# Performance work log

Measured on AMD Instinct MI355X. Metric: run time of the kernel, lower is better.

The kernel has to match this reference:

```python
import jax, jax.numpy as jnp
import numpy as np

NUM_HEADS = 4
NUM_GROUPS = 8
EPS = 1e-5


def group_norm(x, w, b):
    # x: (B, C, H, W); normalize per group of C//NUM_GROUPS channels
    B, C, H, W = x.shape
    xg = x.reshape(B, NUM_GROUPS, C // NUM_GROUPS, H, W)
    mean = xg.mean(axis=(2, 3, 4), keepdims=True)
    var = xg.var(axis=(2, 3, 4), keepdims=True)
    xn = ((xg - mean) * jax.lax.rsqrt(var + EPS)).reshape(B, C, H, W)
    return xn * w[None, :, None, None] + b[None, :, None, None]


def conv1x1(x, w, b):
    # x: (B, C_in, H, W), w: (C_out, C_in), b: (C_out,)
    return jnp.einsum('bchw,oc->bohw', x, w) + b[None, :, None, None]


def setup_inputs() -> dict:
    key = jax.random.key(0)
    B, C, H, W = 4, 256, 64, 64
    k1, k2, k3 = jax.random.split(key, 3)
    scale = 1.0 / np.sqrt(C)
    return {
        'x': jax.random.normal(k1, (B, C, H, W), dtype=jnp.float32),
        'norm_w': jnp.ones((C,), dtype=jnp.float32),
        'norm_b': jnp.zeros((C,), dtype=jnp.float32),
        'qkv_w': jax.random.normal(k2, (3 * C, C), dtype=jnp.float32) * scale,
        'qkv_b': jnp.zeros((3 * C,), dtype=jnp.float32),
        'proj_w': jax.random.normal(k3, (C, C), dtype=jnp.float32) * scale,
        'proj_b': jnp.zeros((C,), dtype=jnp.float32),
    }


def reference(x, norm_w, norm_b, qkv_w, qkv_b, proj_w, proj_b):
    B, C, H, W = x.shape
    hd = C // NUM_HEADS  # head dim
    h = group_norm(x, norm_w, norm_b)
    qkv = conv1x1(h, qkv_w, qkv_b)            # (B, 3C, H, W)
    q, k, v = jnp.split(qkv, 3, axis=1)
    q = q.reshape(B, NUM_HEADS, hd, H * W)
    k = k.reshape(B, NUM_HEADS, hd, H * W)
    v = v.reshape(B, NUM_HEADS, hd, H * W)
    attn = jnp.einsum('bhcn,bhcm->bhnm', q, k) / jnp.sqrt(jnp.asarray(hd, x.dtype))
    attn = jax.nn.softmax(attn, axis=-1)
    out = jnp.einsum('bhnm,bhcm->bhcn', attn, v).reshape(B, C, H, W)
    out = conv1x1(out, proj_w, proj_b)
    return x + out
```

## Files before the change

kernel.cpp:

```cpp
#include <hip/hip_runtime.h>
#include <hip/hip_bf16.h>
#include <stdint.h>


#define B_  4
#define C_  256
#define N_  4096
#define NH_ 4
#define HD_ 64
#define G_  8
#define CPG_ 32
#define GRP_ELEMS (CPG_ * N_)

typedef __attribute__((ext_vector_type(8))) short short8;
typedef __attribute__((ext_vector_type(4))) float f32x4;
typedef __attribute__((ext_vector_type(4))) unsigned short us4;

__device__ __forceinline__ unsigned short f2bf(float f) {
  union { float f; unsigned u; } v; v.f = f;
  unsigned r = v.u + 0x7FFFu + ((v.u >> 16) & 1u);
  return (unsigned short)(r >> 16);
}

__device__ __forceinline__ unsigned pkbf2(float a, float b) {
  __hip_bfloat162 h = __float22bfloat162_rn(make_float2(a, b));
  unsigned r; __builtin_memcpy(&r, &h, sizeof(r)); return r;
}

__device__ __forceinline__ void dma16(const unsigned short* g, unsigned short* l) {
  __builtin_amdgcn_global_load_lds(
      (const __attribute__((address_space(1))) unsigned int*)(g),
      (__attribute__((address_space(3))) unsigned int*)(l), 16, 0, 0);
}

__global__ void gn_partial_cvt(const float* __restrict__ x, float* __restrict__ partial,
                               const float* __restrict__ qkvw, const float* __restrict__ projw,
                               unsigned short* __restrict__ wq, unsigned short* __restrict__ wp) {
  __shared__ float ls[8];
  int t = threadIdx.x;
  if (blockIdx.x >= 512) {
    int i = (blockIdx.x - 512) * 256 + t;
    if (i < 768 * 256) wq[i] = f2bf(qkvw[i]);
    if (i < 256 * 256) wp[i] = f2bf(projw[i]);
    return;
  }
  int idx = blockIdx.x;
  int slice = idx & 15, g = (idx >> 4) & 7, b = idx >> 7;
  const float* base = x + (size_t)(b * C_ + g * CPG_) * N_ + slice * 256;
  float s = 0.f, sq = 0.f;
#pragma unroll
  for (int cc = 0; cc < CPG_; cc++) {
    float v = base[(size_t)cc * N_ + t];
    s += v; sq += v * v;
  }
#pragma unroll
  for (int off = 32; off; off >>= 1) {
    s  += __shfl_down(s,  off, 64);
    sq += __shfl_down(sq, off, 64);
  }
  int wave = t >> 6, lane = t & 63;
  if (lane == 0) { ls[wave * 2] = s; ls[wave * 2 + 1] = sq; }
  __syncthreads();
  if (t == 0) {
    float S = ls[0] + ls[2] + ls[4] + ls[6];
    float SQ = ls[1] + ls[3] + ls[5] + ls[7];
    partial[idx * 2] = S; partial[idx * 2 + 1] = SQ;
  }
}

__global__ void gn_apply(const float* __restrict__ x,
                         const float* __restrict__ nw, const float* __restrict__ nb,
                         const float* __restrict__ partial, unsigned short* __restrict__ hT) {
  int nt = blockIdx.x, ct = blockIdx.y, b = blockIdx.z;
  __shared__ unsigned short tile[32][72];
  int t = threadIdx.x;
  int lane = t & 63;
  int grp = b * G_ + ct;
  float s = 0.f, sq = 0.f;
  if (lane < 16) {
    s  = partial[(grp * 16 + lane) * 2];
    sq = partial[(grp * 16 + lane) * 2 + 1];
  }
#pragma unroll
  for (int off = 8; off; off >>= 1) {
    s  += __shfl_down(s,  off, 64);
    sq += __shfl_down(sq, off, 64);
  }
  s  = __shfl(s,  0, 64);
  sq = __shfl(sq, 0, 64);
  const float inv = 1.0f / (float)GRP_ELEMS;
  float mean = s * inv;
  float rstd = rsqrtf(sq * inv - mean * mean + 1e-5f);

  int n_loc = t & 63, c_loc = t >> 6;
  const float* xb = x + (size_t)(b * C_ + ct * CPG_) * N_ + nt * 64;
#pragma unroll
  for (int rr = 0; rr < 8; rr++) {
    int cc = rr * 4 + c_loc;
    int c = ct * CPG_ + cc;
    float v = xb[(size_t)cc * N_ + n_loc];
    v = (v - mean) * rstd * nw[c] + nb[c];
    tile[cc][n_loc] = f2bf(v);
  }
  __syncthreads();
  int c2 = t & 31, n2 = t >> 5;
  unsigned short* out = hT + ((size_t)(b * N_ + nt * 64)) * C_ + ct * CPG_ + c2;
#pragma unroll
  for (int pass = 0; pass < 8; pass++) {
    int n = pass * 8 + n2;
    out[(size_t)n * C_] = tile[c2][n];
  }
}

__global__ __launch_bounds__(256) void qkv_gemm(
    const unsigned short* __restrict__ hT, const unsigned short* __restrict__ wq,
    const float* __restrict__ qb,
    unsigned short* __restrict__ Qt, unsigned short* __restrict__ Kt,
    unsigned short* __restrict__ V) {
  int ot = blockIdx.x >> 7;
  int nt = (blockIdx.x & 127) >> 2;
  int b  = blockIdx.x & 3;
  int t = threadIdx.x;
  int wave = t >> 6, lane = t & 63, l15 = lane & 15, quad = lane >> 4, l7 = l15 & 7;
  int o_base = ot * 64 + wave * 16;

  __shared__ __align__(16) unsigned short sh[128 * C_];
  {
    int row0 = wave * 2 + (lane >> 5);
    int col8 = lane & 31;
    int src8 = (col8 & 24) | ((col8 & 7) ^ (row0 & 7));
    const unsigned short* gsrc = hT + ((size_t)(b * N_ + nt * 128 + row0)) * C_ + src8 * 8;
#pragma unroll
    for (int it = 0; it < 16; it++)
      dma16(gsrc + (size_t)it * 8 * C_, sh + (it * 8 + wave * 2) * C_);
  }

  f32x4 acc[8];
#pragma unroll
  for (int tt = 0; tt < 8; tt++) acc[tt] = (f32x4){0.f, 0.f, 0.f, 0.f};

  const short8* arow = reinterpret_cast<const short8*>(wq + (size_t)(o_base + l15) * C_);

  asm volatile("s_waitcnt vmcnt(0)" ::: "memory");
  __syncthreads();

#pragma unroll
  for (int kk = 0; kk < 8; kk++) {
    short8 a = arow[kk * 4 + quad];
    int g = kk * 4 + quad;
    int col8 = (g & 24) | ((g & 7) ^ l7);
#pragma unroll
    for (int tt = 0; tt < 8; tt++) {
      short8 bf = *reinterpret_cast<const short8*>(&sh[(tt * 16 + l15) * C_ + col8 * 8]);
      acc[tt] = __builtin_amdgcn_mfma_f32_16x16x32_bf16(a, bf, acc[tt], 0, 0, 0);
    }
  }

  int sec = ot >> 2, head = ot & 3;
  int cw = wave * 16 + quad * 4;
  int bh = b * NH_ + head;
  const float SC = 0.125f * 1.44269504088896340736f;

  if (sec == 0) {
#pragma unroll
    for (int tt = 0; tt < 8; tt++) {
      int n = nt * 128 + tt * 16 + l15;
      us4 pk;
#pragma unroll
      for (int i = 0; i < 4; i++)
        pk[i] = f2bf((acc[tt][i] + qb[ot * 64 + cw + i]) * SC);
      *reinterpret_cast<us4*>(Qt + ((size_t)bh * N_ + n) * HD_ + cw) = pk;
    }
  } else if (sec == 1) {
#pragma unroll
    for (int tt = 0; tt < 8; tt++) {
      int n = nt * 128 + tt * 16 + l15;
      us4 pk;
#pragma unroll
      for (int i = 0; i < 4; i++)
        pk[i] = f2bf(acc[tt][i] + qb[ot * 64 + cw + i]);
      *reinterpret_cast<us4*>(Kt + ((size_t)bh * N_ + n) * HD_ + cw) = pk;
    }
  } else {
#pragma unroll
    for (int tt = 0; tt < 8; tt++) {
      int n = nt * 128 + tt * 16 + l15;
#pragma unroll
      for (int i = 0; i < 4; i++)
        V[((size_t)bh * HD_ + cw + i) * N_ + n] = f2bf(acc[tt][i] + qb[ot * 64 + cw + i]);
    }
  }
}

__global__ __launch_bounds__(256, 2) void flash_attn(
    const unsigned short* __restrict__ Qt, const unsigned short* __restrict__ Kt,
    const unsigned short* __restrict__ Vv, unsigned short* __restrict__ aoT) {
  int bh = blockIdx.x & 15, qt = blockIdx.x >> 4;
  int b = bh >> 2, head = bh & 3;
  int t = threadIdx.x;
  int wave = t >> 6, lane = t & 63, l15 = lane & 15, quad = lane >> 4;
  int l7 = l15 & 7;
  int qsub = wave >> 1, khalf = wave & 1;

  const unsigned short* Qb = Qt + (size_t)bh * N_ * HD_;
  const unsigned short* Kb = Kt + (size_t)bh * N_ * HD_;
  const unsigned short* Vb = Vv + (size_t)bh * HD_ * N_;
  int q_base = qt * 128 + qsub * 64;

  __shared__ __align__(16) unsigned char smem[74752];
  unsigned short* Ks = (unsigned short*)smem;
  unsigned short* Vs = (unsigned short*)(smem + 32768);
  unsigned short* Ps = (unsigned short*)(smem + 65536);
  float* Obuf = (float*)smem;
  float* lbuf = (float*)(smem + 34816);

  const short8 vones = {(short)0x3F80, (short)0x3F80, (short)0x3F80, (short)0x3F80,
                        (short)0x3F80, (short)0x3F80, (short)0x3F80, (short)0x3F80};

  short8 qf[4][2];
#pragma unroll
  for (int r = 0; r < 4; r++)
#pragma unroll
    for (int h = 0; h < 2; h++)
      qf[r][h] = *reinterpret_cast<const short8*>(
          Qb + (size_t)(q_base + r * 16 + l15) * HD_ + h * 32 + quad * 8);

  f32x4 oa[4][4], la[4];
#pragma unroll
  for (int r = 0; r < 4; r++) {
    la[r] = (f32x4){0.f, 0.f, 0.f, 0.f};
#pragma unroll
    for (int ct = 0; ct < 4; ct++) oa[r][ct] = (f32x4){0.f, 0.f, 0.f, 0.f};
  }

  int i8 = lane >> 3, e = lane & 7;
  int perm = (e ^ i8) * 8;
  int kvoff = (khalf * 2) * 4096;
  auto stage = [&](int kt2, int buf) {
    int m0 = khalf * 2048 + kt2 * 64;
    unsigned short* Kd = Ks + kvoff + buf * 4096;
    unsigned short* Vd = Vs + kvoff + buf * 4096;
#pragma unroll
    for (int cc = 0; cc < 4; cc++) {
      int c = qsub * 4 + cc;
      dma16(Kb + (size_t)(m0 + c * 8 + i8) * HD_ + perm, Kd + c * 512);
      dma16(Vb + (size_t)(c * 8 + i8) * N_ + m0 + perm, Vd + c * 512);
    }
  };

  stage(0, 0);

  unsigned short* Pw = Ps + wave * 16 * 72;

#pragma unroll 1
  for (int kt = 0; kt < 32; kt++) {
    int buf = kt & 1;
    if (kt + 1 < 32) {
      stage(kt + 1, buf ^ 1);
      asm volatile("s_waitcnt vmcnt(8)" ::: "memory");
    } else {
      asm volatile("s_waitcnt vmcnt(0)" ::: "memory");
    }
    __builtin_amdgcn_s_barrier();

    const unsigned short* Kbuf = Ks + kvoff + buf * 4096;
    const unsigned short* Vbuf = Vs + kvoff + buf * 4096;

    short8 kf[4][2], vf[4][2];
#pragma unroll
    for (int tt = 0; tt < 4; tt++)
#pragma unroll
      for (int kh2 = 0; kh2 < 2; kh2++) {
        kf[tt][kh2] = *reinterpret_cast<const short8*>(
            &Kbuf[(tt * 16 + l15) * 64 + (((kh2 * 4 + quad) ^ l7) * 8)]);
        vf[tt][kh2] = *reinterpret_cast<const short8*>(
            &Vbuf[(tt * 16 + l15) * 64 + (((kh2 * 4 + quad) ^ l7) * 8)]);
      }

#pragma unroll
    for (int r = 0; r < 4; r++) {
      f32x4 s[4];
#pragma unroll
      for (int tt = 0; tt < 4; tt++) {
        f32x4 z = (f32x4){0.f, 0.f, 0.f, 0.f};
        z = __builtin_amdgcn_mfma_f32_16x16x32_bf16(kf[tt][0], qf[r][0], z, 0, 0, 0);
        s[tt] = __builtin_amdgcn_mfma_f32_16x16x32_bf16(kf[tt][1], qf[r][1], z, 0, 0, 0);
      }
#pragma unroll
      for (int tt = 0; tt < 4; tt++) {
        union { unsigned u2[2]; us4 v; } w;
        w.u2[0] = pkbf2(__builtin_amdgcn_exp2f(s[tt][0]), __builtin_amdgcn_exp2f(s[tt][1]));
        w.u2[1] = pkbf2(__builtin_amdgcn_exp2f(s[tt][2]), __builtin_amdgcn_exp2f(s[tt][3]));
        *reinterpret_cast<us4*>(&Pw[l15 * 72 + tt * 16 + quad * 4]) = w.v;
      }
      short8 pf0 = *reinterpret_cast<const short8*>(&Pw[l15 * 72 + quad * 8]);
      short8 pf1 = *reinterpret_cast<const short8*>(&Pw[l15 * 72 + 32 + quad * 8]);
#pragma unroll
      for (int ct = 0; ct < 4; ct++) {
        oa[r][ct] = __builtin_amdgcn_mfma_f32_16x16x32_bf16(vf[ct][0], pf0, oa[r][ct], 0, 0, 0);
        oa[r][ct] = __builtin_amdgcn_mfma_f32_16x16x32_bf16(vf[ct][1], pf1, oa[r][ct], 0, 0, 0);
      }
      la[r] = __builtin_amdgcn_mfma_f32_16x16x32_bf16(vones, pf0, la[r], 0, 0, 0);
      la[r] = __builtin_amdgcn_mfma_f32_16x16x32_bf16(vones, pf1, la[r], 0, 0, 0);
    }
  }

  __builtin_amdgcn_s_barrier();
  if (khalf == 1) {
#pragma unroll
    for (int r = 0; r < 4; r++) {
#pragma unroll
      for (int ct = 0; ct < 4; ct++)
#pragma unroll
        for (int i = 0; i < 4; i++)
          Obuf[qsub * 4352 + (ct * 16 + quad * 4 + i) * 68 + r * 16 + l15] = oa[r][ct][i];
      if (quad == 0) lbuf[qsub * 64 + r * 16 + l15] = la[r][0];
    }
  }
  __builtin_amdgcn_s_barrier();
  if (khalf == 0) {
#pragma unroll
    for (int r = 0; r < 4; r++) {
      float inv = 1.0f / (la[r][0] + lbuf[qsub * 64 + r * 16 + l15]);
      int n = q_base + r * 16 + l15;
#pragma unroll
      for (int ct = 0; ct < 4; ct++) {
        const float* ob = &Obuf[qsub * 4352 + (ct * 16 + quad * 4) * 68 + r * 16 + l15];
        union { unsigned u2[2]; us4 v; } w;
        w.u2[0] = pkbf2((oa[r][ct][0] + ob[0]) * inv, (oa[r][ct][1] + ob[68]) * inv);
        w.u2[1] = pkbf2((oa[r][ct][2] + ob[136]) * inv, (oa[r][ct][3] + ob[204]) * inv);
        *reinterpret_cast<us4*>(
            aoT + ((size_t)(b * N_ + n)) * C_ + head * HD_ + ct * 16 + quad * 4) = w.v;
      }
    }
  }
}

__global__ __launch_bounds__(256) void proj_gemm(
    const unsigned short* __restrict__ aoT, const unsigned short* __restrict__ wp,
    const float* __restrict__ pb, const float* __restrict__ x,
    float* __restrict__ out) {
  int ot = blockIdx.x >> 7;
  int nt = (blockIdx.x & 127) >> 2;
  int b  = blockIdx.x & 3;
  int t = threadIdx.x;
  int wave = t >> 6, lane = t & 63, l15 = lane & 15, quad = lane >> 4, l7 = l15 & 7;
  int o_base = ot * 64 + wave * 16;

  __shared__ __align__(16) unsigned short sh[128 * C_];
  {
    int row0 = wave * 2 + (lane >> 5);
    int col8 = lane & 31;
    int src8 = (col8 & 24) | ((col8 & 7) ^ (row0 & 7));
    const unsigned short* gsrc = aoT + ((size_t)(b * N_ + nt * 128 + row0)) * C_ + src8 * 8;
#pragma unroll
    for (int it = 0; it < 16; it++)
      dma16(gsrc + (size_t)it * 8 * C_, sh + (it * 8 + wave * 2) * C_);
  }

  f32x4 acc[8];
#pragma unroll
  for (int tt = 0; tt < 8; tt++) acc[tt] = (f32x4){0.f, 0.f, 0.f, 0.f};

  const short8* arow = reinterpret_cast<const short8*>(wp + (size_t)(o_base + l15) * C_);

  asm volatile("s_waitcnt vmcnt(0)" ::: "memory");
  __syncthreads();

#pragma unroll
  for (int kk = 0; kk < 8; kk++) {
    short8 a = arow[kk * 4 + quad];
    int g = kk * 4 + quad;
    int col8 = (g & 24) | ((g & 7) ^ l7);
#pragma unroll
    for (int tt = 0; tt < 8; tt++) {
      short8 bf = *reinterpret_cast<const short8*>(&sh[(tt * 16 + l15) * C_ + col8 * 8]);
      acc[tt] = __builtin_amdgcn_mfma_f32_16x16x32_bf16(a, bf, acc[tt], 0, 0, 0);
    }
  }
#pragma unroll
  for (int tt = 0; tt < 8; tt++) {
    int n = nt * 128 + tt * 16 + l15;
#pragma unroll
    for (int i = 0; i < 4; i++) {
      int o = o_base + quad * 4 + i;
      size_t idx = ((size_t)(b * C_ + o)) * N_ + n;
      out[idx] = acc[tt][i] + pb[o] + x[idx];
    }
  }
}

extern "C" void kernel_launch(void* const* d_in, const int* in_sizes, int n_in,
                              void* d_out, int out_size, void* d_ws, size_t ws_size,
                              hipStream_t stream) {
  const float* x      = (const float*)d_in[0];
  const float* norm_w = (const float*)d_in[1];
  const float* norm_b = (const float*)d_in[2];
  const float* qkv_w  = (const float*)d_in[3];
  const float* qkv_b  = (const float*)d_in[4];
  const float* proj_w = (const float*)d_in[5];
  const float* proj_b = (const float*)d_in[6];
  float* out = (float*)d_out;

  char* ws = (char*)d_ws;
  size_t off = 0;
  auto alloc = [&](size_t bytes) { size_t o = off; off = (off + bytes + 255) & ~(size_t)255; return o; };
  size_t off_partial = alloc(512 * 2 * sizeof(float));
  size_t off_stats   = alloc(32 * 2 * sizeof(float));
  size_t off_wq      = alloc((size_t)768 * 256 * 2);
  size_t off_wp      = alloc((size_t)256 * 256 * 2);
  size_t off_hT      = alloc((size_t)B_ * N_ * C_ * 2);
  size_t off_Qt      = alloc((size_t)B_ * NH_ * N_ * HD_ * 2);
  size_t off_Kt      = alloc((size_t)B_ * NH_ * N_ * HD_ * 2);
  size_t off_V       = alloc((size_t)B_ * NH_ * HD_ * N_ * 2);
  size_t off_aoT     = alloc((size_t)B_ * N_ * C_ * 2);
  (void)off_stats;

  float* partial = (float*)(ws + off_partial);
  unsigned short* wq  = (unsigned short*)(ws + off_wq);
  unsigned short* wp  = (unsigned short*)(ws + off_wp);
  unsigned short* hT  = (unsigned short*)(ws + off_hT);
  unsigned short* Qt  = (unsigned short*)(ws + off_Qt);
  unsigned short* Kt  = (unsigned short*)(ws + off_Kt);
  unsigned short* V   = (unsigned short*)(ws + off_V);
  unsigned short* aoT = (unsigned short*)(ws + off_aoT);

  gn_partial_cvt<<<1280, 256, 0, stream>>>(x, partial, qkv_w, proj_w, wq, wp);
  gn_apply<<<dim3(64, 8, 4), 256, 0, stream>>>(x, norm_w, norm_b, partial, hT);
  qkv_gemm<<<1536, 256, 0, stream>>>(hT, wq, qkv_b, Qt, Kt, V);
  flash_attn<<<512, 256, 0, stream>>>(Qt, Kt, V, aoT);
  proj_gemm<<<512, 256, 0, stream>>>(aoT, wp, proj_b, x, out);
}
```

Baseline: 193.3 us.

## Double QKV GEMM output tile per block and vectorize gn_apply stores

The QKV GEMM now computes 128 output channels per block instead of 64, with each wave handling two 16-row A fragments that share B fragments read once from LDS. This halves the grid and the number of redundant hT tile loads into shared memory. In exchange it uses more accumulator registers per thread. Separately, gn_apply's transposed write-out now has each thread emit 8 contiguous bf16 values as two 8-byte stores instead of scattered 2-byte stores.

```diff
diff --git a/kernel.cpp b/kernel.cpp
--- a/kernel.cpp
+++ b/kernel.cpp
@@ -103,13 +103,15 @@
     tile[cc][n_loc] = f2bf(v);
   }
   __syncthreads();
-  int c2 = t & 31, n2 = t >> 5;
-  unsigned short* out = hT + ((size_t)(b * N_ + nt * 64)) * C_ + ct * CPG_ + c2;
-#pragma unroll
-  for (int pass = 0; pass < 8; pass++) {
-    int n = pass * 8 + n2;
-    out[(size_t)n * C_] = tile[c2][n];
-  }
+  int n = t >> 2, c8 = (t & 3) * 8;
+  us4 lo, hi;
+#pragma unroll
+  for (int j = 0; j < 4; j++) lo[j] = tile[c8 + j][n];
+#pragma unroll
+  for (int j = 0; j < 4; j++) hi[j] = tile[c8 + 4 + j][n];
+  unsigned short* outp = hT + ((size_t)(b * N_ + nt * 64 + n)) * C_ + ct * CPG_ + c8;
+  *reinterpret_cast<us4*>(outp) = lo;
+  *reinterpret_cast<us4*>(outp + 4) = hi;
 }
 
 __global__ __launch_bounds__(256) void qkv_gemm(
@@ -122,7 +124,6 @@
   int b  = blockIdx.x & 3;
   int t = threadIdx.x;
   int wave = t >> 6, lane = t & 63, l15 = lane & 15, quad = lane >> 4, l7 = l15 & 7;
-  int o_base = ot * 64 + wave * 16;
 
   __shared__ __align__(16) unsigned short sh[128 * C_];
   {
@@ -135,59 +136,76 @@
       dma16(gsrc + (size_t)it * 8 * C_, sh + (it * 8 + wave * 2) * C_);
   }
 
-  f32x4 acc[8];
-#pragma unroll
-  for (int tt = 0; tt < 8; tt++) acc[tt] = (f32x4){0.f, 0.f, 0.f, 0.f};
-
-  const short8* arow = reinterpret_cast<const short8*>(wq + (size_t)(o_base + l15) * C_);
+  f32x4 acc[2][8];
+#pragma unroll
+  for (int r = 0; r < 2; r++)
+#pragma unroll
+    for (int tt = 0; tt < 8; tt++) acc[r][tt] = (f32x4){0.f, 0.f, 0.f, 0.f};
+
+  const short8* arow[2];
+#pragma unroll
+  for (int r = 0; r < 2; r++)
+    arow[r] = reinterpret_cast<const short8*>(
+        wq + (size_t)(ot * 128 + wave * 32 + r * 16 + l15) * C_);
 
   asm volatile("s_waitcnt vmcnt(0)" ::: "memory");
   __syncthreads();
 
 #pragma unroll
   for (int kk = 0; kk < 8; kk++) {
-    short8 a = arow[kk * 4 + quad];
     int g = kk * 4 + quad;
     int col8 = (g & 24) | ((g & 7) ^ l7);
-#pragma unroll
-    for (int tt = 0; tt < 8; tt++) {
-      short8 bf = *reinterpret_cast<const short8*>(&sh[(tt * 16 + l15) * C_ + col8 * 8]);
-      acc[tt] = __builtin_amdgcn_mfma_f32_16x16x32_bf16(a, bf, acc[tt], 0, 0, 0);
-    }
-  }
-
-  int sec = ot >> 2, head = ot & 3;
-  int cw = wave * 16 + quad * 4;
+    short8 bfr[8];
+#pragma unroll
+    for (int tt = 0; tt < 8; tt++)
+      bfr[tt] = *reinterpret_cast<const short8*>(&sh[(tt * 16 + l15) * C_ + col8 * 8]);
+#pragma unroll
+    for (int r = 0; r < 2; r++) {
+      short8 a = arow[r][g];
+#pragma unroll
+      for (int tt = 0; tt < 8; tt++)
+        acc[r][tt] = __builtin_amdgcn_mfma_f32_16x16x32_bf16(a, bfr[tt], acc[r][tt], 0, 0, 0);
+    }
+  }
+
+  int sec = ot >> 1;
+  int head = (ot & 1) * 2 + (wave >> 1);
   int bh = b * NH_ + head;
   const float SC = 0.125f * 1.44269504088896340736f;
 
-  if (sec == 0) {
-#pragma unroll
-    for (int tt = 0; tt < 8; tt++) {
-      int n = nt * 128 + tt * 16 + l15;
-      us4 pk;
-#pragma unroll
-      for (int i = 0; i < 4; i++)
-        pk[i] = f2bf((acc[tt][i] + qb[ot * 64 + cw + i]) * SC);
-      *reinterpret_cast<us4*>(Qt + ((size_t)bh * N_ + n) * HD_ + cw) = pk;
-    }
-  } else if (sec == 1) {
-#pragma unroll
-    for (int tt = 0; tt < 8; tt++) {
-      int n = nt * 128 + tt * 16 + l15;
-      us4 pk;
-#pragma unroll
-      for (int i = 0; i < 4; i++)
-        pk[i] = f2bf(acc[tt][i] + qb[ot * 64 + cw + i]);
-      *reinterpret_cast<us4*>(Kt + ((size_t)bh * N_ + n) * HD_ + cw) = pk;
-    }
-  } else {
-#pragma unroll
-    for (int tt = 0; tt < 8; tt++) {
-      int n = nt * 128 + tt * 16 + l15;
-#pragma unroll
-      for (int i = 0; i < 4; i++)
-        V[((size_t)bh * HD_ + cw + i) * N_ + n] = f2bf(acc[tt][i] + qb[ot * 64 + cw + i]);
+#pragma unroll
+  for (int r = 0; r < 2; r++) {
+    int o_glob = ot * 128 + wave * 32 + r * 16;
+    int cw = (o_glob & 63) + quad * 4;
+    if (sec == 0) {
+#pragma unroll
+      for (int tt = 0; tt < 8; tt++) {
+        int n = nt * 128 + tt * 16 + l15;
+        us4 pk;
+#pragma unroll
+        for (int i = 0; i < 4; i++)
+          pk[i] = f2bf((acc[r][tt][i] + qb[o_glob + quad * 4 + i]) * SC);
+        *reinterpret_cast<us4*>(Qt + ((size_t)bh * N_ + n) * HD_ + cw) = pk;
+      }
+    } else if (sec == 1) {
+#pragma unroll
+      for (int tt = 0; tt < 8; tt++) {
+        int n = nt * 128 + tt * 16 + l15;
+        us4 pk;
+#pragma unroll
+        for (int i = 0; i < 4; i++)
+          pk[i] = f2bf(acc[r][tt][i] + qb[o_glob + quad * 4 + i]);
+        *reinterpret_cast<us4*>(Kt + ((size_t)bh * N_ + n) * HD_ + cw) = pk;
+      }
+    } else {
+#pragma unroll
+      for (int tt = 0; tt < 8; tt++) {
+        int n = nt * 128 + tt * 16 + l15;
+#pragma unroll
+        for (int i = 0; i < 4; i++)
+          V[((size_t)bh * HD_ + cw + i) * N_ + n] =
+              f2bf(acc[r][tt][i] + qb[o_glob + quad * 4 + i]);
+      }
     }
   }
 }
@@ -427,7 +445,7 @@
 
   gn_partial_cvt<<<1280, 256, 0, stream>>>(x, partial, qkv_w, proj_w, wq, wp);
   gn_apply<<<dim3(64, 8, 4), 256, 0, stream>>>(x, norm_w, norm_b, partial, hT);
-  qkv_gemm<<<1536, 256, 0, stream>>>(hT, wq, qkv_b, Qt, Kt, V);
+  qkv_gemm<<<768, 256, 0, stream>>>(hT, wq, qkv_b, Qt, Kt, V);
   flash_attn<<<512, 256, 0, stream>>>(Qt, Kt, V, aoT);
   proj_gemm<<<512, 256, 0, stream>>>(aoT, wp, proj_b, x, out);
 }
```

Result: no change. 192.5 us (-0.4%).
